# Kernel tuning notes

Measured on AMD Instinct MI355X. Metric: run time of the kernel, lower is better.

The kernel has to match this reference:

```python
import jax, jax.numpy as jnp
import numpy as np

N_NODES = 100000
N_EDGES = 3200000
D_FEAT = 64
CLAMP = 20.0
POSINF = 1.0e6
NEGINF = -1.0e6


def setup_inputs() -> dict:
    key = jax.random.key(0)
    k1, k2, k3, k4 = jax.random.split(key, 4)
    x = jax.random.normal(k1, (N_NODES, D_FEAT), dtype=jnp.float32)
    edge_src = jax.random.randint(k2, (N_EDGES,), 0, N_NODES, dtype=jnp.int64 if jax.config.jax_enable_x64 else jnp.int32).astype(jnp.int32)
    edge_dst = jax.random.randint(k3, (N_EDGES,), 0, N_NODES, dtype=jnp.int32)
    # symmetric-normalized-adjacency-like positive weights
    edge_w = jax.random.uniform(k4, (N_EDGES,), dtype=jnp.float32)
    t = jnp.zeros((1,), dtype=jnp.float32)
    return {"t": t, "x": x, "edge_src": edge_src, "edge_dst": edge_dst, "edge_w": edge_w}


def reference(t, x, edge_src, edge_dst, edge_w):
    # out = sparse.mm(G, x): out[dst] += w * x[src]  (COO SpMM via segment_sum)
    msgs = edge_w[:, None] * x[edge_src]                 # [E, d]
    out = jax.ops.segment_sum(msgs, edge_dst, num_segments=N_NODES)  # [N, d]
    # numerical_stability epilogue: nan/inf sanitize + clamp
    out = jnp.nan_to_num(out, nan=0.0, posinf=POSINF, neginf=NEGINF)
    out = jnp.clip(out, -CLAMP, CLAMP)
    return out
```

## Files before the change

### kernel.cpp

```cpp
#include <hip/hip_runtime.h>
#include <hip/hip_fp16.h>
#include <math.h>

#define N_NODES 100000
#define N_EDGES 3200000
#define D_FEAT  64
#define CLAMP_V 20.0f

#define BSH 6
#define BSZ 64
#define NB  1563
#define SBNSH 10
#define NSB 98
#define CPAD 32
#define CHUNKP 4096
#define NCHUNK ((N_EDGES + CHUNKP - 1) / CHUNKP)
#define CAPL 2560
#define HISTB 512
#define NSLC 4
#define NBIN 256


__global__ __launch_bounds__(256)
void prep_kernel(const float4* __restrict__ xin, ushort4* __restrict__ xh,
                 const int* __restrict__ edst, int* __restrict__ counts,
                 int n4) {
    __shared__ int h[NSB];
    if (blockIdx.x < HISTB) {
        if (threadIdx.x < NSB) h[threadIdx.x] = 0;
        __syncthreads();
        const int4* d4p = (const int4*)edst;
        int total4 = N_EDGES >> 2;
        for (int i = blockIdx.x * blockDim.x + threadIdx.x; i < total4;
             i += HISTB * blockDim.x) {
            int4 d4 = d4p[i];
            atomicAdd(&h[d4.x >> SBNSH], 1);
            atomicAdd(&h[d4.y >> SBNSH], 1);
            atomicAdd(&h[d4.z >> SBNSH], 1);
            atomicAdd(&h[d4.w >> SBNSH], 1);
        }
        __syncthreads();
        if (threadIdx.x < NSB) {
            int v = h[threadIdx.x];
            if (v) atomicAdd(&counts[threadIdx.x * CPAD], v);
        }
    } else {
        int i = (blockIdx.x - HISTB) * blockDim.x + threadIdx.x;
        if (i < n4) {
            float4 v = xin[i];
            ushort4 o;
            o.x = __half_as_ushort(__float2half(v.x));
            o.y = __half_as_ushort(__float2half(v.y));
            o.z = __half_as_ushort(__float2half(v.z));
            o.w = __half_as_ushort(__float2half(v.w));
            xh[i] = o;
        }
    }
}

__global__ void scan_kernel(const int* __restrict__ counts,
                            int* __restrict__ bstartsSB,
                            int* __restrict__ cursors1) {
    __shared__ int wtot[2];
    int t = threadIdx.x;
    int lane = t & 63, wv = t >> 6;
    int c = (t < NSB) ? counts[t * CPAD] : 0;
    int sc = c;
#pragma unroll
    for (int off = 1; off < 64; off <<= 1) {
        int u = __shfl_up(sc, off);
        if (lane >= off) sc += u;
    }
    if (lane == 63) wtot[wv] = sc;
    __syncthreads();
    int base = (wv == 1) ? wtot[0] : 0;
    int excl = base + sc - c;
    if (t < NSB) {
        bstartsSB[t] = excl;
        cursors1[t * CPAD] = excl;
    }
    if (t == 0) bstartsSB[NSB] = N_EDGES;
}

__global__ __launch_bounds__(512)
void pass1_kernel(const int* __restrict__ esrc,
                  const int* __restrict__ edst,
                  const float* __restrict__ ew,
                  int* __restrict__ cursors1,
                  unsigned* __restrict__ rk32,
                  unsigned short* __restrict__ ra16) {
    __shared__ unsigned       spk[CHUNKP];
    __shared__ unsigned short sax[CHUNKP];
    __shared__ unsigned char  binof[CHUNKP];
    __shared__ int h[NSB];
    __shared__ int hstart[NSB];
    __shared__ int lcur[NSB];
    __shared__ int lbase[NSB];
    __shared__ int wtot[2];

    int c0   = blockIdx.x * CHUNKP;
    int cend = min(c0 + CHUNKP, N_EDGES);
    int n    = cend - c0;
    int nv   = n >> 2;
    const int4*   d4p = (const int4*)(edst + c0);
    const int4*   s4p = (const int4*)(esrc + c0);
    const float4* w4p = (const float4*)(ew + c0);
    int t = threadIdx.x;

    if (t < NSB) h[t] = 0;
    __syncthreads();
    for (int i = t; i < nv; i += 512) {
        int4 d4 = d4p[i];
        atomicAdd(&h[d4.x >> SBNSH], 1);
        atomicAdd(&h[d4.y >> SBNSH], 1);
        atomicAdd(&h[d4.z >> SBNSH], 1);
        atomicAdd(&h[d4.w >> SBNSH], 1);
    }
    __syncthreads();
    int c = 0, sc = 0;
    if (t < 128) {
        c = (t < NSB) ? h[t] : 0;
        sc = c;
#pragma unroll
        for (int off = 1; off < 64; off <<= 1) {
            int u = __shfl_up(sc, off);
            if ((t & 63) >= off) sc += u;
        }
        if ((t & 63) == 63) wtot[t >> 6] = sc;
    }
    __syncthreads();
    if (t < NSB) {
        int base = (t >= 64) ? wtot[0] : 0;
        int excl = base + sc - c;
        hstart[t] = excl;
        lcur[t]   = excl;
        lbase[t]  = c ? atomicAdd(&cursors1[t * CPAD], c) : 0;
    }
    __syncthreads();
    for (int i = t; i < nv; i += 512) {
        int4   d4 = d4p[i];
        int4   s4 = s4p[i];
        float4 w4 = w4p[i];
#define PUT(dd, ss, ww)                                                       \
        {                                                                     \
            int bk  = (dd) >> SBNSH;                                          \
            int pos = atomicAdd(&lcur[bk], 1);                                \
            unsigned hw = __half_as_ushort(__float2half(ww));                 \
            spk[pos] = ((hw & 0xFFFEu) << 16) | (unsigned)(ss);               \
            sax[pos] = (unsigned short)((dd) & 1023);                         \
            binof[pos] = (unsigned char)bk;                                   \
        }
        PUT(d4.x, s4.x, w4.x);
        PUT(d4.y, s4.y, w4.y);
        PUT(d4.z, s4.z, w4.z);
        PUT(d4.w, s4.w, w4.w);
#undef PUT
    }
    __syncthreads();
    for (int i = t; i < n; i += 512) {
        int bk = binof[i];
        int o  = lbase[bk] + (i - hstart[bk]);
        rk32[o] = spk[i];
        ra16[o] = sax[i];
    }
}

__global__ __launch_bounds__(512)
void sort_gather_kernel(const __half* __restrict__ xh,
                        const unsigned* __restrict__ rk32,
                        const unsigned short* __restrict__ ra16,
                        const int* __restrict__ bstartsSB,
                        float* __restrict__ out) {
    __shared__ unsigned      sbuf[CAPL];
    __shared__ unsigned      stg[CAPL];
    __shared__ unsigned char sbin[CAPL];
    __shared__ int h[NBIN + 1];
    __shared__ int cur[NBIN];
    __shared__ int wsum4[4];
    __shared__ int mcnt;
    int t    = threadIdx.x;
    int lane = t & 63;
    int wv   = t >> 6;
    int g    = lane >> 4;
    int s    = lane & 15;
    const char* xbase = (const char*)xh + (s << 3);

    int b    = blockIdx.x;
    int sbid = b >> 4;
    int fk   = b & 15;
    int sbeg = bstartsSB[sbid];
    int send = bstartsSB[sbid + 1];

    if (t <= NBIN) h[t] = 0;
    if (t == 0) mcnt = 0;
    __syncthreads();
    int a0 = sbeg & ~3;
    for (int i0 = a0 + t * 4; i0 < send; i0 += 512 * 4) {
        int4    r4 = *(const int4*)(rk32 + i0);
        ushort4 a4 = *(const ushort4*)(ra16 + i0);
#define FILT(J, RR, AA)                                                       \
        {                                                                     \
            int idx = i0 + (J);                                               \
            if (idx >= sbeg && idx < send && (int)((AA) >> 6) == fk) {        \
                int bin = (int)((((unsigned)(RR) >> 15) & 3u) << 6)           \
                        | (int)((AA) & 63u);                                  \
                int pos = atomicAdd(&mcnt, 1);                                \
                if (pos < CAPL) {                                             \
                    stg[pos]  = (unsigned)(RR);                               \
                    sbin[pos] = (unsigned char)bin;                           \
                    atomicAdd(&h[bin + 1], 1);                                \
                }                                                             \
            }                                                                 \
        }
        FILT(0, r4.x, a4.x);
        FILT(1, r4.y, a4.y);
        FILT(2, r4.z, a4.z);
        FILT(3, r4.w, a4.w);
#undef FILT
    }
    __syncthreads();
    int cnt = mcnt;
    if (cnt > CAPL) cnt = CAPL;
    if (t < NBIN) {
        int sc = h[t + 1];
#pragma unroll
        for (int off = 1; off < 64; off <<= 1) {
            int u = __shfl_up(sc, off);
            if (lane >= off) sc += u;
        }
        if (lane == 63) wsum4[wv] = sc;
        __syncthreads();
        if (t == 0) {
            int r = 0;
#pragma unroll
            for (int j = 0; j < 4; ++j) { int v = wsum4[j]; wsum4[j] = r; r += v; }
        }
        __syncthreads();
        h[t + 1] = sc + wsum4[wv];
    } else {
        __syncthreads();
        __syncthreads();
    }
    __syncthreads();
    if (t < NBIN) cur[t] = h[t];
    __syncthreads();
    for (int e = t; e < cnt; e += 512) {
        sbuf[atomicAdd(&cur[sbin[e]], 1)] = stg[e];
    }
    __syncthreads();

#define GSTEP(EE, K)                                                         \
    {                                                                        \
        unsigned p = sbuf[(EE) + g];                                         \
        float wf = __half2float(__ushort_as_half(                            \
                       (unsigned short)((p >> 16) & 0xFFFEu)));              \
        const ushort4 xv = *(const ushort4*)(xbase +                         \
                       ((size_t)((p & 0x1FFFFu) << 7)));                     \
        ak0[K] = fmaf(__half2float(__ushort_as_half(xv.x)), wf, ak0[K]);     \
        ak1[K] = fmaf(__half2float(__ushort_as_half(xv.y)), wf, ak1[K]);     \
        ak2[K] = fmaf(__half2float(__ushort_as_half(xv.z)), wf, ak2[K]);     \
        ak3[K] = fmaf(__half2float(__ushort_as_half(xv.w)), wf, ak3[K]);     \
    }
#define GSTEPC(EE, S1, K)                                                    \
    {                                                                        \
        int eg = (EE) + g;                                                   \
        unsigned p = sbuf[eg < (S1) ? eg : ((S1) - 1)];                      \
        float wf = (eg < (S1)) ? __half2float(__ushort_as_half(              \
                       (unsigned short)((p >> 16) & 0xFFFEu))) : 0.0f;       \
        const ushort4 xv = *(const ushort4*)(xbase +                         \
                       ((size_t)((p & 0x1FFFFu) << 7)));                     \
        ak0[K] = fmaf(__half2float(__ushort_as_half(xv.x)), wf, ak0[K]);     \
        ak1[K] = fmaf(__half2float(__ushort_as_half(xv.y)), wf, ak1[K]);     \
        ak2[K] = fmaf(__half2float(__ushort_as_half(xv.z)), wf, ak2[K]);     \
        ak3[K] = fmaf(__half2float(__ushort_as_half(xv.w)), wf, ak3[K]);     \
    }

    int node0 = b << BSH;
    float ak0[8], ak1[8], ak2[8], ak3[8];
#pragma unroll
    for (int k = 0; k < 8; ++k) { ak0[k] = 0.f; ak1[k] = 0.f; ak2[k] = 0.f; ak3[k] = 0.f; }
#pragma unroll 1
    for (int blk = 0; blk < NSLC; ++blk) {
#pragma unroll
        for (int k = 0; k < 8; ++k) {
            int seg = (blk << 6) | ((wv << 3) + k);
            int s0 = h[seg];
            int s1 = h[seg + 1];
            int e = s0;
            for (; e + 8 <= s1; e += 8) {
                GSTEP(e, k);
                GSTEP(e + 4, k);
            }
            for (; e + 4 <= s1; e += 4)
                GSTEP(e, k);
            if (e < s1)
                GSTEPC(e, s1, k);
        }
    }
#pragma unroll
    for (int k = 0; k < 8; ++k) {
        float a0 = ak0[k], a1 = ak1[k], a2 = ak2[k], a3 = ak3[k];
        a0 += __shfl_xor(a0, 16); a0 += __shfl_xor(a0, 32);
        a1 += __shfl_xor(a1, 16); a1 += __shfl_xor(a1, 32);
        a2 += __shfl_xor(a2, 16); a2 += __shfl_xor(a2, 32);
        a3 += __shfl_xor(a3, 16); a3 += __shfl_xor(a3, 32);
        if (isnan(a0)) a0 = 0.0f;
        if (isnan(a1)) a1 = 0.0f;
        if (isnan(a2)) a2 = 0.0f;
        if (isnan(a3)) a3 = 0.0f;
        a0 = fminf(fmaxf(a0, -CLAMP_V), CLAMP_V);
        a1 = fminf(fmaxf(a1, -CLAMP_V), CLAMP_V);
        a2 = fminf(fmaxf(a2, -CLAMP_V), CLAMP_V);
        a3 = fminf(fmaxf(a3, -CLAMP_V), CLAMP_V);
        int node = node0 + (wv << 3) + k;
        if (lane < 16 && node < N_NODES)
            *(float4*)(out + ((size_t)node << 6) + (s << 2)) =
                make_float4(a0, a1, a2, a3);
    }
#undef GSTEP
#undef GSTEPC
}

__global__ void zero_kernel(float4* __restrict__ out, int n4) {
    int i = blockIdx.x * blockDim.x + threadIdx.x;
    if (i < n4) out[i] = make_float4(0.f, 0.f, 0.f, 0.f);
}

__global__ void scatter_kernel(const float* __restrict__ x,
                               const int* __restrict__ esrc,
                               const int* __restrict__ edst,
                               const float* __restrict__ ew,
                               float* __restrict__ out) {
    long long tid = (long long)blockIdx.x * blockDim.x + threadIdx.x;
    int edge = (int)(tid >> 4);
    int q    = (int)(tid & 15);
    if (edge >= N_EDGES) return;
    int   s = esrc[edge];
    int   d = edst[edge];
    float w = ew[edge];
    const float4* xrow = (const float4*)(x + (size_t)s * D_FEAT);
    float4 v = xrow[q];
    float* orow = out + (size_t)d * D_FEAT + q * 4;
    atomicAdd(orow + 0, w * v.x);
    atomicAdd(orow + 1, w * v.y);
    atomicAdd(orow + 2, w * v.z);
    atomicAdd(orow + 3, w * v.w);
}

__global__ void epilogue_kernel(float4* __restrict__ out, int n4) {
    int i = blockIdx.x * blockDim.x + threadIdx.x;
    if (i >= n4) return;
    float4 v = out[i];
    float* p = &v.x;
#pragma unroll
    for (int k = 0; k < 4; ++k) {
        float f = p[k];
        if (isnan(f)) f = 0.0f;
        f = fminf(fmaxf(f, -CLAMP_V), CLAMP_V);
        p[k] = f;
    }
    out[i] = v;
}

extern "C" void kernel_launch(void* const* d_in, const int* in_sizes, int n_in,
                              void* d_out, int out_size, void* d_ws, size_t ws_size,
                              hipStream_t stream) {
    const float* x    = (const float*)d_in[1];
    const int*   esrc = (const int*)d_in[2];
    const int*   edst = (const int*)d_in[3];
    const float* ew   = (const float*)d_in[4];
    float*       out  = (float*)d_out;

    size_t meta_ints = (size_t)NSB * CPAD
                     + (NSB + 1)
                     + (size_t)NSB * CPAD;
    meta_ints = (meta_ints + 3) & ~(size_t)3;
    size_t rk_bytes  = (size_t)N_EDGES * sizeof(unsigned);
    size_t ra_bytes  = (size_t)N_EDGES * sizeof(unsigned short);
    size_t xh_bytes  = (size_t)N_NODES * D_FEAT * sizeof(__half);
    size_t need = meta_ints * sizeof(int) + rk_bytes + ra_bytes + xh_bytes;

    if (ws_size >= need) {
        int*      counts    = (int*)d_ws;
        int*      bstartsSB = counts + (size_t)NSB * CPAD;
        int*      cursors1  = bstartsSB + (NSB + 1);
        unsigned* rk32      = (unsigned*)((int*)d_ws + meta_ints);
        unsigned short* ra16 = (unsigned short*)((char*)rk32 + rk_bytes);
        __half*   xh        = (__half*)((char*)ra16 + ra_bytes);

        hipMemsetAsync(counts, 0, (size_t)NSB * CPAD * sizeof(int), stream);
        {
            int n4 = N_NODES * D_FEAT / 4;
            prep_kernel<<<HISTB + (n4 + 255) / 256, 256, 0, stream>>>(
                (const float4*)x, (ushort4*)xh, edst, counts, n4);
        }
        scan_kernel<<<1, 128, 0, stream>>>(counts, bstartsSB, cursors1);
        pass1_kernel<<<NCHUNK, 512, 0, stream>>>(esrc, edst, ew, cursors1,
                                                 rk32, ra16);
        sort_gather_kernel<<<NB, 512, 0, stream>>>(xh, rk32, ra16, bstartsSB,
                                                   out);
    } else {
        const int n4 = N_NODES * D_FEAT / 4;
        zero_kernel<<<(n4 + 255) / 256, 256, 0, stream>>>((float4*)out, n4);
        long long total = (long long)N_EDGES * 16;
        scatter_kernel<<<(int)((total + 255) / 256), 256, 0, stream>>>(x, esrc, edst, ew, out);
        epilogue_kernel<<<(n4 + 255) / 256, 256, 0, stream>>>((float4*)out, n4);
    }
}
```

Baseline: 238.5 us.

## Replace staging buffer with two-pass histogram scatter and remap block order

```diff
diff --git a/kernel.cpp b/kernel.cpp
--- a/kernel.cpp
+++ b/kernel.cpp
@@ -19,6 +19,8 @@
 #define HISTB 512
 #define NSLC 4
 #define NBIN 256
+#define GRIDSG 1568
+#define CPX (GRIDSG / 8)
 
 
 __global__ __launch_bounds__(256)
@@ -171,13 +173,10 @@
                         const unsigned short* __restrict__ ra16,
                         const int* __restrict__ bstartsSB,
                         float* __restrict__ out) {
-    __shared__ unsigned      sbuf[CAPL];
-    __shared__ unsigned      stg[CAPL];
-    __shared__ unsigned char sbin[CAPL];
+    __shared__ unsigned sbuf[CAPL];
     __shared__ int h[NBIN + 1];
     __shared__ int cur[NBIN];
     __shared__ int wsum4[4];
-    __shared__ int mcnt;
     int t    = threadIdx.x;
     int lane = t & 63;
     int wv   = t >> 6;
@@ -185,42 +184,36 @@
     int s    = lane & 15;
     const char* xbase = (const char*)xh + (s << 3);
 
-    int b    = blockIdx.x;
+    int p = blockIdx.x;
+    int b = (p & 7) * CPX + (p >> 3);
+    if (b >= NB) return;
     int sbid = b >> 4;
     int fk   = b & 15;
     int sbeg = bstartsSB[sbid];
     int send = bstartsSB[sbid + 1];
 
     if (t <= NBIN) h[t] = 0;
-    if (t == 0) mcnt = 0;
     __syncthreads();
     int a0 = sbeg & ~3;
     for (int i0 = a0 + t * 4; i0 < send; i0 += 512 * 4) {
+        ushort4 a4 = *(const ushort4*)(ra16 + i0);
         int4    r4 = *(const int4*)(rk32 + i0);
-        ushort4 a4 = *(const ushort4*)(ra16 + i0);
-#define FILT(J, RR, AA)                                                       \
+#define FILTH(J, RR, AA)                                                      \
         {                                                                     \
             int idx = i0 + (J);                                               \
             if (idx >= sbeg && idx < send && (int)((AA) >> 6) == fk) {        \
                 int bin = (int)((((unsigned)(RR) >> 15) & 3u) << 6)           \
                         | (int)((AA) & 63u);                                  \
-                int pos = atomicAdd(&mcnt, 1);                                \
-                if (pos < CAPL) {                                             \
-                    stg[pos]  = (unsigned)(RR);                               \
-                    sbin[pos] = (unsigned char)bin;                           \
-                    atomicAdd(&h[bin + 1], 1);                                \
-                }                                                             \
+                atomicAdd(&h[bin + 1], 1);                                    \
             }                                                                 \
         }
-        FILT(0, r4.x, a4.x);
-        FILT(1, r4.y, a4.y);
-        FILT(2, r4.z, a4.z);
-        FILT(3, r4.w, a4.w);
-#undef FILT
-    }
-    __syncthreads();
-    int cnt = mcnt;
-    if (cnt > CAPL) cnt = CAPL;
+        FILTH(0, r4.x, a4.x);
+        FILTH(1, r4.y, a4.y);
+        FILTH(2, r4.z, a4.z);
+        FILTH(3, r4.w, a4.w);
+#undef FILTH
+    }
+    __syncthreads();
     if (t < NBIN) {
         int sc = h[t + 1];
 #pragma unroll
@@ -236,7 +229,7 @@
             for (int j = 0; j < 4; ++j) { int v = wsum4[j]; wsum4[j] = r; r += v; }
         }
         __syncthreads();
-        h[t + 1] = sc + wsum4[wv];
+        h[t + 1] = min(sc + wsum4[wv], CAPL);
     } else {
         __syncthreads();
         __syncthreads();
@@ -244,18 +237,34 @@
     __syncthreads();
     if (t < NBIN) cur[t] = h[t];
     __syncthreads();
-    for (int e = t; e < cnt; e += 512) {
-        sbuf[atomicAdd(&cur[sbin[e]], 1)] = stg[e];
+    for (int i0 = a0 + t * 4; i0 < send; i0 += 512 * 4) {
+        ushort4 a4 = *(const ushort4*)(ra16 + i0);
+        int4    r4 = *(const int4*)(rk32 + i0);
+#define FILTP(J, RR, AA)                                                      \
+        {                                                                     \
+            int idx = i0 + (J);                                               \
+            if (idx >= sbeg && idx < send && (int)((AA) >> 6) == fk) {        \
+                int bin = (int)((((unsigned)(RR) >> 15) & 3u) << 6)           \
+                        | (int)((AA) & 63u);                                  \
+                int pos = atomicAdd(&cur[bin], 1);                            \
+                if (pos < CAPL) sbuf[pos] = (unsigned)(RR);                   \
+            }                                                                 \
+        }
+        FILTP(0, r4.x, a4.x);
+        FILTP(1, r4.y, a4.y);
+        FILTP(2, r4.z, a4.z);
+        FILTP(3, r4.w, a4.w);
+#undef FILTP
     }
     __syncthreads();
 
 #define GSTEP(EE, K)                                                         \
     {                                                                        \
-        unsigned p = sbuf[(EE) + g];                                         \
+        unsigned p2 = sbuf[(EE) + g];                                        \
         float wf = __half2float(__ushort_as_half(                            \
-                       (unsigned short)((p >> 16) & 0xFFFEu)));              \
+                       (unsigned short)((p2 >> 16) & 0xFFFEu)));             \
         const ushort4 xv = *(const ushort4*)(xbase +                         \
-                       ((size_t)((p & 0x1FFFFu) << 7)));                     \
+                       ((size_t)((p2 & 0x1FFFFu) << 7)));                    \
         ak0[K] = fmaf(__half2float(__ushort_as_half(xv.x)), wf, ak0[K]);     \
         ak1[K] = fmaf(__half2float(__ushort_as_half(xv.y)), wf, ak1[K]);     \
         ak2[K] = fmaf(__half2float(__ushort_as_half(xv.z)), wf, ak2[K]);     \
@@ -264,11 +273,11 @@
 #define GSTEPC(EE, S1, K)                                                    \
     {                                                                        \
         int eg = (EE) + g;                                                   \
-        unsigned p = sbuf[eg < (S1) ? eg : ((S1) - 1)];                      \
+        unsigned p2 = sbuf[eg < (S1) ? eg : ((S1) - 1)];                     \
         float wf = (eg < (S1)) ? __half2float(__ushort_as_half(              \
-                       (unsigned short)((p >> 16) & 0xFFFEu))) : 0.0f;       \
+                       (unsigned short)((p2 >> 16) & 0xFFFEu))) : 0.0f;      \
         const ushort4 xv = *(const ushort4*)(xbase +                         \
-                       ((size_t)((p & 0x1FFFFu) << 7)));                     \
+                       ((size_t)((p2 & 0x1FFFFu) << 7)));                    \
         ak0[K] = fmaf(__half2float(__ushort_as_half(xv.x)), wf, ak0[K]);     \
         ak1[K] = fmaf(__half2float(__ushort_as_half(xv.y)), wf, ak1[K]);     \
         ak2[K] = fmaf(__half2float(__ushort_as_half(xv.z)), wf, ak2[K]);     \
@@ -397,8 +406,8 @@
         scan_kernel<<<1, 128, 0, stream>>>(counts, bstartsSB, cursors1);
         pass1_kernel<<<NCHUNK, 512, 0, stream>>>(esrc, edst, ew, cursors1,
                                                  rk32, ra16);
-        sort_gather_kernel<<<NB, 512, 0, stream>>>(xh, rk32, ra16, bstartsSB,
-                                                   out);
+        sort_gather_kernel<<<GRIDSG, 512, 0, stream>>>(xh, rk32, ra16,
+                                                       bstartsSB, out);
     } else {
         const int n4 = N_NODES * D_FEAT / 4;
         zero_kernel<<<(n4 + 255) / 256, 256, 0, stream>>>((float4*)out, n4);
```

Result: slower. 258.4 us (+8.4%).
